# Kernel tuning notes

Measured on AMD Instinct MI355X. Metric: run time of the kernel, lower is better.

The kernel has to match this reference:

```python
import jax, jax.numpy as jnp
import numpy as np

EPS = 1e-12  # torch F.normalize default eps


def setup_inputs() -> dict:
    key = jax.random.key(0)
    ks = jax.random.split(key, 5)
    b, c, h, w = 2, 192, 256, 256
    x = jax.random.normal(ks[0], (b, c, h, w), dtype=jnp.float32)
    temperature = jnp.ones((1, 1, 1), dtype=jnp.float32)
    qkv_w = jax.random.normal(ks[1], (3 * c, c), dtype=jnp.float32) * 0.02
    qkv_b = jax.random.normal(ks[2], (3 * c,), dtype=jnp.float32) * 0.02
    proj_w = jax.random.normal(ks[3], (c, c), dtype=jnp.float32) * 0.02
    proj_b = jax.random.normal(ks[4], (c,), dtype=jnp.float32) * 0.02
    return {"x": x, "temperature": temperature, "qkv_w": qkv_w, "qkv_b": qkv_b,
            "proj_w": proj_w, "proj_b": proj_b}


def reference(x, temperature, qkv_w, qkv_b, proj_w, proj_b):
    b, c, h, w = x.shape
    n = h * w
    # [b, c, h, w] -> [b, n, c] tokens over spatial, features = channels
    xt = x.reshape(b, c, n).transpose(0, 2, 1)
    qkv = xt @ qkv_w.T + qkv_b                     # [b, n, 3c]
    q, k, v = jnp.split(qkv, 3, axis=-1)           # each [b, n, c]
    q = q.transpose(0, 2, 1)                       # [b, c, n]
    k = k.transpose(0, 2, 1)
    v = v.transpose(0, 2, 1)
    # L2 normalize along spatial (last) dim, torch-style clamp
    q = q / jnp.maximum(jnp.linalg.norm(q, axis=-1, keepdims=True), EPS)
    k = k / jnp.maximum(jnp.linalg.norm(k, axis=-1, keepdims=True), EPS)
    attn = jnp.einsum('bcn,bdn->bcd', q, k) * temperature[0, 0, 0]  # [b, c, c]
    attn = jax.nn.softmax(attn, axis=-1)
    out = jnp.einsum('bcd,bdn->bcn', attn, v)      # [b, c, n]
    out = out.reshape(b, c, h, w)
    # 1x1 conv projection = channel matmul
    out = jnp.einsum('bchw,dc->bdhw', out, proj_w) + proj_b[None, :, None, None]
    return out
```

## Files before the change

kernel.cpp:

```cpp
#include <hip/hip_runtime.h>
#include <hip/hip_bf16.h>
#include <stdint.h>

typedef __attribute__((ext_vector_type(8))) __bf16 bf16x8;
typedef __attribute__((ext_vector_type(4))) float f32x4;
typedef __attribute__((ext_vector_type(4))) uint u32x4;

#define C192 192
#define NSP 65536
#define EPS_N 1e-12f

#define SLICE_ELEMS 20224
#define ONES_OFF_E 19968

__device__ __forceinline__ uint32_t f2bf1(float a){
  uint32_t u = __float_as_uint(a);
  return (u + 0x7fffu + ((u >> 16) & 1u)) >> 16;
}
__device__ __forceinline__ uint32_t f2bf2(float lo, float hi){
  return f2bf1(lo) | (f2bf1(hi) << 16);
}
__device__ __forceinline__ float bf2f(ushort u){
  return __uint_as_float(((uint32_t)u) << 16);
}

__global__ __launch_bounds__(384, 2) void k_gram(const float* __restrict__ x,
                                                 ushort* __restrict__ gpart){
  __shared__ ushort xs[192 * 128];
  char* lb = (char*)xs;
  const int tid = threadIdx.x;
  const int lane = tid & 63, wid = tid >> 6;
  const int l15 = lane & 15, hi = lane >> 4;
  const int b = blockIdx.x >> 9, slice = blockIdx.x & 511;
  const int j0 = slice * 128;

  const int rA = wid, rB = 11 - wid, nA = 13 - rA;

  const float* xg = x + ((size_t)b * C192) * NSP + j0;

  float4 rf[16];
  #pragma unroll
  for (int u = 0; u < 8; u++){
    int unit = u * 384 + tid;
    int row = unit >> 4, u16 = unit & 15;
    const float* src = xg + (size_t)row * NSP + u16 * 8;
    rf[2 * u]     = *(const float4*)(src);
    rf[2 * u + 1] = *(const float4*)(src + 4);
  }
  #pragma unroll
  for (int u = 0; u < 8; u++){
    int unit = u * 384 + tid;
    int row = unit >> 4, u16 = unit & 15;
    uint4 v;
    v.x = f2bf2(rf[2 * u].x,     rf[2 * u].y);
    v.y = f2bf2(rf[2 * u].z,     rf[2 * u].w);
    v.z = f2bf2(rf[2 * u + 1].x, rf[2 * u + 1].y);
    v.w = f2bf2(rf[2 * u + 1].z, rf[2 * u + 1].w);
    int byte = row * 256 + u16 * 16; byte ^= (row & 7) << 4;
    *(uint4*)(lb + byte) = v;
  }

  f32x4 acc[15];
  #pragma unroll
  for (int t = 0; t < 15; t++) acc[t] = (f32x4){0.f, 0.f, 0.f, 0.f};

  __syncthreads();

  uint ov = (l15 == 0) ? 0x3F803F80u : 0u;
  u32x4 oq = {ov, ov, ov, ov};
  bf16x8 onesf = __builtin_bit_cast(bf16x8, oq);
  #pragma unroll
  for (int ks = 0; ks < 4; ks++){
    bf16x8 aA, aB;
    { int byte = (rA * 16 + l15) * 256 + ks * 64 + hi * 16; byte ^= (l15 & 7) << 4;
      aA = *(const bf16x8*)(lb + byte); }
    { int byte = (rB * 16 + l15) * 256 + ks * 64 + hi * 16; byte ^= (l15 & 7) << 4;
      aB = *(const bf16x8*)(lb + byte); }
    #pragma unroll
    for (int t = 0; t < 15; t++){
      int j = (t < nA) ? (rA + t) : (rB + t - nA);
      bf16x8 bf;
      if (j < 12){
        int byte = (j * 16 + l15) * 256 + ks * 64 + hi * 16; byte ^= (l15 & 7) << 4;
        bf = *(const bf16x8*)(lb + byte);
      } else {
        bf = onesf;
      }
      acc[t] = __builtin_amdgcn_mfma_f32_16x16x32_bf16((t < nA) ? aA : aB, bf, acc[t], 0, 0, 0);
    }
  }

  ushort* gp = gpart + (size_t)(b * 512 + slice) * SLICE_ELEMS;
  #pragma unroll
  for (int t = 0; t < 15; t++){
    int i = (t < nA) ? rA : rB;
    int j = (t < nA) ? (rA + t) : (rB + t - nA);
    uint2 u2;
    u2.x = f2bf2(acc[t][0], acc[t][1]);
    u2.y = f2bf2(acc[t][2], acc[t][3]);
    if (j < 12){
      int F = 12 * i - (i * (i - 1)) / 2 + (j - i);
      *(uint2*)(gp + F * 256 + lane * 4) = u2;
    } else if (l15 == 0){
      *(uint2*)(gp + ONES_OFF_E + i * 16 + hi * 4) = u2;
    }
  }
}

__global__ __launch_bounds__(1024) void k_reduce(const ushort* __restrict__ gpart,
                                                 float* __restrict__ gaug,
                                                 const float* __restrict__ qkv_w,
                                                 float* __restrict__ wkT){
  int blk = blockIdx.x, tid = threadIdx.x;
  if (blk < 180){
    __shared__ float red[4][256];
    int b = blk / 90, slot = blk % 90;
    int q = tid >> 8, e = tid & 255;
    float sum = 0.f;
    if (slot < 78){
      const ushort* p = gpart + (size_t)(b * 512 + q) * SLICE_ELEMS + slot * 256 + e;
      #pragma unroll 8
      for (int k2 = 0; k2 < 128; k2++) sum += bf2f(p[(size_t)k2 * (4 * SLICE_ELEMS)]);
    } else if (e < 16){
      int i = slot - 78;
      const ushort* p = gpart + (size_t)(b * 512 + q) * SLICE_ELEMS + ONES_OFF_E + i * 16 + e;
      #pragma unroll 8
      for (int k2 = 0; k2 < 128; k2++) sum += bf2f(p[(size_t)k2 * (4 * SLICE_ELEMS)]);
    }
    red[q][e] = sum;
    __syncthreads();
    if (tid < 256){
      float tot = red[0][tid] + red[1][tid] + red[2][tid] + red[3][tid];
      if (slot < 78){
        int i = 0, off = 0;
        while (slot >= off + (12 - i)){ off += 12 - i; i++; }
        int j = i + (slot - off);
        int e2 = tid;
        int row = ((e2 >> 6) << 2) | (e2 & 3);
        int col = (e2 >> 2) & 15;
        int R = i * 16 + row, Cc = j * 16 + col;
        gaug[((size_t)b * C192 + R) * 193 + Cc] = tot;
        gaug[((size_t)b * C192 + Cc) * 193 + R] = tot;
      } else if (tid < 16){
        int i = slot - 78;
        gaug[((size_t)b * C192 + i * 16 + tid) * 193 + 192] = tot;
      }
    }
  } else {
    int idx = (blk - 180) * 1024 + tid;
    if (idx < 36864){
      int d = idx / 192, e = idx % 192;
      wkT[e * 192 + d] = qkv_w[(192 + d) * 192 + e];
    }
  }
}

__global__ __launch_bounds__(256) void k_pr(const float* __restrict__ gaug,
                                            const float* __restrict__ qkv_w,
                                            const float* __restrict__ qkv_b,
                                            float* __restrict__ pr,
                                            float* __restrict__ norms){
  __shared__ float red[4];
  __shared__ float uSh;
  int blk = blockIdx.x, tid = threadIdx.x;
  int b = blk / 384, which = (blk / 192) % 2, c = blk % 192;
  const float* wrow = qkv_w + (which * 192 + c) * 192;
  float acc = 0.f;
  if (tid < 193){
    const float* g = gaug + (size_t)b * C192 * 193 + tid;
    #pragma unroll 4
    for (int e = 0; e < 192; e++) acc += wrow[e] * g[(size_t)e * 193];
    pr[(((size_t)b * 2 + which) * 192 + c) * 193 + tid] = acc;
  }
  if (tid == 192) uSh = acc;
  float v = (tid < 192) ? acc * wrow[tid] : 0.f;
  for (int o = 32; o > 0; o >>= 1) v += __shfl_down(v, o, 64);
  if ((tid & 63) == 0) red[tid >> 6] = v;
  __syncthreads();
  if (tid == 0){
    float s = red[0] + red[1] + red[2] + red[3];
    float bias = qkv_b[which * 192 + c];
    float n2 = s + 2.f * bias * uSh + 65536.f * bias * bias;
    norms[(b * 2 + which) * 192 + c] = fmaxf(sqrtf(fmaxf(n2, 0.f)), EPS_N);
  }
}

__global__ __launch_bounds__(256) void k_attn_u(const float* __restrict__ pr,
                                                const float* __restrict__ wkT,
                                                const float* __restrict__ norms,
                                                const float* __restrict__ qkv_b,
                                                const float* __restrict__ temperature,
                                                const float* __restrict__ qkv_w,
                                                float* __restrict__ uaug){
  __shared__ float Pc[193];
  __shared__ float red[4];
  __shared__ float bcast;
  int blk = blockIdx.x, tid = threadIdx.x;
  int b = blk / 192, c = blk % 192;
  if (tid < 193) Pc[tid] = pr[(((size_t)b * 2 + 0) * 192 + c) * 193 + tid];
  __syncthreads();
  int d = tid;
  float logit = -1e30f, p = 0.f;
  if (d < 192){
    float sS = 0.f;
    #pragma unroll 4
    for (int e = 0; e < 192; e++) sS += Pc[e] * wkT[e * 192 + d];
    float bq = qkv_b[c], bk = qkv_b[192 + d];
    float w2 = pr[(((size_t)b * 2 + 1) * 192 + d) * 193 + 192];
    float Sv = sS + Pc[192] * bk + bq * w2 + 65536.f * bq * bk;
    float nq = norms[(b * 2 + 0) * 192 + c];
    float nk = norms[(b * 2 + 1) * 192 + d];
    logit = temperature[0] * Sv / (nq * nk);
  }
  float m = logit;
  for (int o = 32; o > 0; o >>= 1) m = fmaxf(m, __shfl_down(m, o, 64));
  if ((tid & 63) == 0) red[tid >> 6] = m;
  __syncthreads();
  if (tid == 0) bcast = fmaxf(fmaxf(red[0], red[1]), fmaxf(red[2], red[3]));
  __syncthreads();
  m = bcast;
  p = (d < 192) ? __expf(logit - m) : 0.f;
  float s = p;
  for (int o = 32; o > 0; o >>= 1) s += __shfl_down(s, o, 64);
  __syncthreads();
  if ((tid & 63) == 0) red[tid >> 6] = s;
  __syncthreads();
  if (tid == 0) bcast = red[0] + red[1] + red[2] + red[3];
  __syncthreads();
  float aw = (d < 192) ? (p / bcast) : 0.f;
  __syncthreads();
  if (d < 192) Pc[d] = aw;
  __syncthreads();
  int e = tid;
  if (e <= 192){
    float acc = 0.f;
    if (e < 192){
      #pragma unroll 4
      for (int d2 = 0; d2 < 192; d2++) acc += Pc[d2] * qkv_w[(384 + d2) * 192 + e];
    } else {
      #pragma unroll 4
      for (int d2 = 0; d2 < 192; d2++) acc += Pc[d2] * qkv_b[384 + d2];
    }
    uaug[((size_t)b * 192 + c) * 193 + e] = acc;
  }
}

__global__ __launch_bounds__(256) void k_f(const float* __restrict__ uaug,
                                           const float* __restrict__ proj_w,
                                           const float* __restrict__ proj_b,
                                           ushort* __restrict__ fb,
                                           float* __restrict__ gvec){
  __shared__ float pw[192];
  int blk = blockIdx.x, tid = threadIdx.x;
  int b = blk / 192, f = blk % 192;
  if (tid < 192) pw[tid] = proj_w[f * 192 + tid];
  __syncthreads();
  int e = tid;
  if (e <= 192){
    float acc = 0.f;
    const float* u = uaug + (size_t)b * 192 * 193 + e;
    #pragma unroll 4
    for (int c2 = 0; c2 < 192; c2++) acc += pw[c2] * u[(size_t)c2 * 193];
    if (e < 192) fb[((size_t)b * 192 + f) * 192 + e] = (ushort)f2bf1(acc);
    else gvec[b * 192 + f] = acc + proj_b[f];
  }
}

__global__ __launch_bounds__(256, 3) void k_out(const float* __restrict__ x,
                                                const ushort* __restrict__ fb,
                                                const float* __restrict__ gvec,
                                                float* __restrict__ out){
  __shared__ ushort xt[128 * 192];
  char* lb = (char*)xt;
  const int tid = threadIdx.x;
  const int lane = tid & 63, wid = tid >> 6;
  const int l15 = lane & 15, hi = lane >> 4;
  const int b = blockIdx.x >> 9, cb = blockIdx.x & 511;
  const int j0 = cb * 128;

  const float* xg = x + ((size_t)b * C192) * NSP + j0;
  #pragma unroll
  for (int half = 0; half < 2; half++){
    float4 ra[12];
    #pragma unroll
    for (int ii = 0; ii < 3; ii++){
      int unit = (half * 3 + ii) * 256 + tid;
      int cp = unit >> 4, s8 = unit & 15;
      int c0 = cp * 2, sp0 = s8 * 8;
      const float* r0 = xg + (size_t)c0 * NSP + sp0;
      const float* r1 = xg + (size_t)(c0 + 1) * NSP + sp0;
      ra[4 * ii]     = *(const float4*)(r0);
      ra[4 * ii + 1] = *(const float4*)(r0 + 4);
      ra[4 * ii + 2] = *(const float4*)(r1);
      ra[4 * ii + 3] = *(const float4*)(r1 + 4);
    }
    #pragma unroll
    for (int ii = 0; ii < 3; ii++){
      int unit = (half * 3 + ii) * 256 + tid;
      int cp = unit >> 4, s8 = unit & 15;
      int c0 = cp * 2, sp0 = s8 * 8;
      float fa[8] = {ra[4*ii].x, ra[4*ii].y, ra[4*ii].z, ra[4*ii].w,
                     ra[4*ii+1].x, ra[4*ii+1].y, ra[4*ii+1].z, ra[4*ii+1].w};
      float fc[8] = {ra[4*ii+2].x, ra[4*ii+2].y, ra[4*ii+2].z, ra[4*ii+2].w,
                     ra[4*ii+3].x, ra[4*ii+3].y, ra[4*ii+3].z, ra[4*ii+3].w};
      #pragma unroll
      for (int s = 0; s < 8; s++){
        int sp = sp0 + s;
        int byte = sp * 384 + c0 * 2;
        byte ^= (((sp & 7) ^ ((sp >> 3) & 7)) << 4);
        *(uint*)(lb + byte) = f2bf2(fa[s], fc[s]);
      }
    }
  }

  float gfr[3][4];
  #pragma unroll
  for (int i = 0; i < 3; i++)
    #pragma unroll
    for (int r = 0; r < 4; r++)
      gfr[i][r] = gvec[b * 192 + (wid * 3 + i) * 16 + hi * 4 + r];

  f32x4 acc[3][8];
  #pragma unroll
  for (int i = 0; i < 3; i++)
    #pragma unroll
    for (int j = 0; j < 8; j++)
      acc[i][j] = (f32x4){0.f, 0.f, 0.f, 0.f};

  __syncthreads();

  for (int w = 0; w < 6; w++){
    bf16x8 aF[3];
    #pragma unroll
    for (int i = 0; i < 3; i++){
      const ushort* fr = fb + ((size_t)b * 192 + (wid * 3 + i) * 16 + l15) * 192;
      aF[i] = *(const bf16x8*)(fr + w * 32 + hi * 8);
    }
    #pragma unroll
    for (int ct = 0; ct < 8; ct++){
      int sp = ct * 16 + l15;
      int byte = sp * 384 + w * 64 + hi * 16;
      byte ^= (((sp & 7) ^ ((sp >> 3) & 7)) << 4);
      bf16x8 bf = *(const bf16x8*)(lb + byte);
      #pragma unroll
      for (int i = 0; i < 3; i++)
        acc[i][ct] = __builtin_amdgcn_mfma_f32_16x16x32_bf16(aF[i], bf, acc[i][ct], 0, 0, 0);
    }
  }

  #pragma unroll
  for (int i = 0; i < 3; i++){
    int row0 = (wid * 3 + i) * 16 + hi * 4;
    #pragma unroll
    for (int ct = 0; ct < 8; ct++){
      int sp = j0 + ct * 16 + l15;
      float* ob = out + ((size_t)b * C192 + row0) * NSP + sp;
      #pragma unroll
      for (int r = 0; r < 4; r++) ob[(size_t)r * NSP] = acc[i][ct][r] + gfr[i][r];
    }
  }
}

extern "C" void kernel_launch(void* const* d_in, const int* in_sizes, int n_in,
                              void* d_out, int out_size, void* d_ws, size_t ws_size,
                              hipStream_t stream){
  const float* x           = (const float*)d_in[0];
  const float* temperature = (const float*)d_in[1];
  const float* qkv_w       = (const float*)d_in[2];
  const float* qkv_b       = (const float*)d_in[3];
  const float* proj_w      = (const float*)d_in[4];
  const float* proj_b      = (const float*)d_in[5];
  float* out = (float*)d_out;
  char* ws = (char*)d_ws;

  ushort* gpart = (ushort*)(ws);
  float*  gaug  = (float*) (ws + 41418752);
  float*  pr    = (float*) (ws + 41715200);
  float*  wkT   = (float*) (ws + 42308096);
  float*  norms = (float*) (ws + 42455552);
  float*  uaug  = (float*) (ws + 42458624);
  ushort* fb    = (ushort*)(ws + 42755072);
  float*  gvec  = (float*) (ws + 42902528);

  hipLaunchKernelGGL(k_gram,   dim3(1024), dim3(384),  0, stream, x, gpart);
  hipLaunchKernelGGL(k_reduce, dim3(216),  dim3(1024), 0, stream, gpart, gaug, qkv_w, wkT);
  hipLaunchKernelGGL(k_pr,     dim3(768),  dim3(256),  0, stream, gaug, qkv_w, qkv_b, pr, norms);
  hipLaunchKernelGGL(k_attn_u, dim3(384),  dim3(256),  0, stream, pr, wkT, norms, qkv_b, temperature, qkv_w, uaug);
  hipLaunchKernelGGL(k_f,      dim3(384),  dim3(256),  0, stream, uaug, proj_w, proj_b, fb, gvec);
  hipLaunchKernelGGL(k_out,    dim3(1024), dim3(256),  0, stream, x, fb, gvec, out);
}
```

Before: 147.7 us.

## Pipeline Gram kernel with async global-to-LDS double buffering over wider slices

The Gram kernel now has each block process a 512-column slice in 16 chunks. Chunks are staged as fp32 into double-buffered LDS via global_load_lds, overlapping loads with MFMA compute, and converted to bf16 at fragment-load time. Work is split across 12 waves instead of 6, and there are 4x fewer partial slices, which shrinks the workspace and the reduce kernel's loop. The trade-offs are a per-chunk barrier, more conversion work per fragment read, fewer total blocks (256), and a higher launch bound that may pressure registers.

```diff
diff --git a/kernel.cpp b/kernel.cpp
--- a/kernel.cpp
+++ b/kernel.cpp
@@ -24,77 +24,81 @@
   return __uint_as_float(((uint32_t)u) << 16);
 }
 
-__global__ __launch_bounds__(384, 2) void k_gram(const float* __restrict__ x,
+__global__ __launch_bounds__(768, 4) void k_gram(const float* __restrict__ x,
                                                  ushort* __restrict__ gpart){
-  __shared__ ushort xs[192 * 128];
+  __shared__ float xs[2 * 6144];
   char* lb = (char*)xs;
   const int tid = threadIdx.x;
   const int lane = tid & 63, wid = tid >> 6;
   const int l15 = lane & 15, hi = lane >> 4;
-  const int b = blockIdx.x >> 9, slice = blockIdx.x & 511;
-  const int j0 = slice * 128;
-
-  const int rA = wid, rB = 11 - wid, nA = 13 - rA;
-
+  const int b = blockIdx.x >> 7, slice = blockIdx.x & 127;
+  const int j0 = slice * 512;
+
+  const int p = (wid < 6) ? wid : (wid - 6);
+  const int nFirst = 5 - p;
   const float* xg = x + ((size_t)b * C192) * NSP + j0;
 
-  float4 rf[16];
-  #pragma unroll
-  for (int u = 0; u < 8; u++){
-    int unit = u * 384 + tid;
-    int row = unit >> 4, u16 = unit & 15;
-    const float* src = xg + (size_t)row * NSP + u16 * 8;
-    rf[2 * u]     = *(const float4*)(src);
-    rf[2 * u + 1] = *(const float4*)(src + 4);
-  }
-  #pragma unroll
-  for (int u = 0; u < 8; u++){
-    int unit = u * 384 + tid;
-    int row = unit >> 4, u16 = unit & 15;
-    uint4 v;
-    v.x = f2bf2(rf[2 * u].x,     rf[2 * u].y);
-    v.y = f2bf2(rf[2 * u].z,     rf[2 * u].w);
-    v.z = f2bf2(rf[2 * u + 1].x, rf[2 * u + 1].y);
-    v.w = f2bf2(rf[2 * u + 1].z, rf[2 * u + 1].w);
-    int byte = row * 256 + u16 * 16; byte ^= (row & 7) << 4;
-    *(uint4*)(lb + byte) = v;
-  }
-
-  f32x4 acc[15];
-  #pragma unroll
-  for (int t = 0; t < 15; t++) acc[t] = (f32x4){0.f, 0.f, 0.f, 0.f};
-
-  __syncthreads();
+  const int swcol = ((lane & 7) ^ (lane >> 3)) * 4;
+  const float* srow = xg + (size_t)(wid * 16 + (lane >> 3)) * NSP + swcol;
+
+  auto ISSUE = [&](int c, int bi){
+    char* dst = lb + bi * 24576 + wid * 2048;
+    const float* s0 = srow + c * 32;
+    const float* s1 = s0 + (size_t)8 * NSP;
+    __builtin_amdgcn_global_load_lds((__attribute__((address_space(1))) const void*)s0,
+                                     (__attribute__((address_space(3))) void*)(dst), 16, 0, 0);
+    __builtin_amdgcn_global_load_lds((__attribute__((address_space(1))) const void*)s1,
+                                     (__attribute__((address_space(3))) void*)(dst + 1024), 16, 0, 0);
+  };
+
+  f32x4 acc[8];
+  #pragma unroll
+  for (int t = 0; t < 8; t++) acc[t] = (f32x4){0.f, 0.f, 0.f, 0.f};
 
   uint ov = (l15 == 0) ? 0x3F803F80u : 0u;
   u32x4 oq = {ov, ov, ov, ov};
   bf16x8 onesf = __builtin_bit_cast(bf16x8, oq);
-  #pragma unroll
-  for (int ks = 0; ks < 4; ks++){
-    bf16x8 aA, aB;
-    { int byte = (rA * 16 + l15) * 256 + ks * 64 + hi * 16; byte ^= (l15 & 7) << 4;
-      aA = *(const bf16x8*)(lb + byte); }
-    { int byte = (rB * 16 + l15) * 256 + ks * 64 + hi * 16; byte ^= (l15 & 7) << 4;
-      aB = *(const bf16x8*)(lb + byte); }
-    #pragma unroll
-    for (int t = 0; t < 15; t++){
-      int j = (t < nA) ? (rA + t) : (rB + t - nA);
-      bf16x8 bf;
-      if (j < 12){
-        int byte = (j * 16 + l15) * 256 + ks * 64 + hi * 16; byte ^= (l15 & 7) << 4;
-        bf = *(const bf16x8*)(lb + byte);
-      } else {
-        bf = onesf;
-      }
-      acc[t] = __builtin_amdgcn_mfma_f32_16x16x32_bf16((t < nA) ? aA : aB, bf, acc[t], 0, 0, 0);
-    }
-  }
-
-  ushort* gp = gpart + (size_t)(b * 512 + slice) * SLICE_ELEMS;
-  #pragma unroll
-  for (int t = 0; t < 15; t++){
-    int i = (t < nA) ? rA : rB;
-    int j = (t < nA) ? (rA + t) : (rB + t - nA);
+
+  auto LOADFRAG = [&](const char* base, int row) -> bf16x8 {
+    int sw = (row & 7) << 4;
+    f32x4 v0 = *(const f32x4*)(base + row * 128 + ((hi * 32) ^ sw));
+    f32x4 v1 = *(const f32x4*)(base + row * 128 + ((hi * 32 + 16) ^ sw));
+    uint w0, w1, w2, w3;
+    asm("v_cvt_pk_bf16_f32 %0, %1, %2" : "=v"(w0) : "v"(v0.x), "v"(v0.y));
+    asm("v_cvt_pk_bf16_f32 %0, %1, %2" : "=v"(w1) : "v"(v0.z), "v"(v0.w));
+    asm("v_cvt_pk_bf16_f32 %0, %1, %2" : "=v"(w2) : "v"(v1.x), "v"(v1.y));
+    asm("v_cvt_pk_bf16_f32 %0, %1, %2" : "=v"(w3) : "v"(v1.z), "v"(v1.w));
+    u32x4 q = {w0, w1, w2, w3};
+    return __builtin_bit_cast(bf16x8, q);
+  };
+
+  auto COMPUTE = [&](int bi){
+    const char* base = lb + bi * 24576;
+    bf16x8 a0 = LOADFRAG(base, p * 16 + l15);
+    bf16x8 a1 = (wid >= 6) ? LOADFRAG(base, (11 - p) * 16 + l15) : a0;
+    #pragma unroll
+    for (int t = 0; t < 8; t++){
+      if (wid >= 6 && t >= 7) break;
+      int j = (wid < 6) ? (p + t) : ((t < nFirst) ? (p + 8 + t) : (t + 6));
+      bf16x8 bf = (j < 12) ? LOADFRAG(base, j * 16 + l15) : onesf;
+      bf16x8 aS = (wid < 6 || t < nFirst) ? a0 : a1;
+      acc[t] = __builtin_amdgcn_mfma_f32_16x16x32_bf16(aS, bf, acc[t], 0, 0, 0);
+    }
+  };
+
+  ISSUE(0, 0);
+  for (int c = 0; c < 16; c++){
+    __syncthreads();
+    if (c < 15) ISSUE(c + 1, (c + 1) & 1);
+    COMPUTE(c & 1);
+  }
+
+  ushort* gp = gpart + (size_t)(b * 128 + slice) * SLICE_ELEMS;
+  #pragma unroll
+  for (int t = 0; t < 8; t++){
+    if (wid >= 6 && t >= 7) break;
+    int i = (wid < 6) ? p : ((t < nFirst) ? p : (11 - p));
+    int j = (wid < 6) ? (p + t) : ((t < nFirst) ? (p + 8 + t) : (t + 6));
     uint2 u2;
     u2.x = f2bf2(acc[t][0], acc[t][1]);
     u2.y = f2bf2(acc[t][2], acc[t][3]);
@@ -118,14 +122,14 @@
     int q = tid >> 8, e = tid & 255;
     float sum = 0.f;
     if (slot < 78){
-      const ushort* p = gpart + (size_t)(b * 512 + q) * SLICE_ELEMS + slot * 256 + e;
+      const ushort* pp = gpart + (size_t)(b * 128 + q) * SLICE_ELEMS + slot * 256 + e;
       #pragma unroll 8
-      for (int k2 = 0; k2 < 128; k2++) sum += bf2f(p[(size_t)k2 * (4 * SLICE_ELEMS)]);
+      for (int k2 = 0; k2 < 32; k2++) sum += bf2f(pp[(size_t)k2 * (4 * SLICE_ELEMS)]);
     } else if (e < 16){
       int i = slot - 78;
-      const ushort* p = gpart + (size_t)(b * 512 + q) * SLICE_ELEMS + ONES_OFF_E + i * 16 + e;
+      const ushort* pp = gpart + (size_t)(b * 128 + q) * SLICE_ELEMS + ONES_OFF_E + i * 16 + e;
       #pragma unroll 8
-      for (int k2 = 0; k2 < 128; k2++) sum += bf2f(p[(size_t)k2 * (4 * SLICE_ELEMS)]);
+      for (int k2 = 0; k2 < 32; k2++) sum += bf2f(pp[(size_t)k2 * (4 * SLICE_ELEMS)]);
     }
     red[q][e] = sum;
     __syncthreads();
@@ -200,7 +204,7 @@
   if (tid < 193) Pc[tid] = pr[(((size_t)b * 2 + 0) * 192 + c) * 193 + tid];
   __syncthreads();
   int d = tid;
-  float logit = -1e30f, p = 0.f;
+  float logit = -1e30f, pv = 0.f;
   if (d < 192){
     float sS = 0.f;
     #pragma unroll 4
@@ -219,15 +223,15 @@
   if (tid == 0) bcast = fmaxf(fmaxf(red[0], red[1]), fmaxf(red[2], red[3]));
   __syncthreads();
   m = bcast;
-  p = (d < 192) ? __expf(logit - m) : 0.f;
-  float s = p;
+  pv = (d < 192) ? __expf(logit - m) : 0.f;
+  float s = pv;
   for (int o = 32; o > 0; o >>= 1) s += __shfl_down(s, o, 64);
   __syncthreads();
   if ((tid & 63) == 0) red[tid >> 6] = s;
   __syncthreads();
   if (tid == 0) bcast = red[0] + red[1] + red[2] + red[3];
   __syncthreads();
-  float aw = (d < 192) ? (p / bcast) : 0.f;
+  float aw = (d < 192) ? (pv / bcast) : 0.f;
   __syncthreads();
   if (d < 192) Pc[d] = aw;
   __syncthreads();
@@ -374,15 +378,15 @@
   char* ws = (char*)d_ws;
 
   ushort* gpart = (ushort*)(ws);
-  float*  gaug  = (float*) (ws + 41418752);
-  float*  pr    = (float*) (ws + 41715200);
-  float*  wkT   = (float*) (ws + 42308096);
-  float*  norms = (float*) (ws + 42455552);
-  float*  uaug  = (float*) (ws + 42458624);
-  ushort* fb    = (ushort*)(ws + 42755072);
-  float*  gvec  = (float*) (ws + 42902528);
-
-  hipLaunchKernelGGL(k_gram,   dim3(1024), dim3(384),  0, stream, x, gpart);
+  float*  gaug  = (float*) (ws + 10354688);
+  float*  pr    = (float*) (ws + 10651136);
+  float*  wkT   = (float*) (ws + 11244032);
+  float*  norms = (float*) (ws + 11391488);
+  float*  uaug  = (float*) (ws + 11394560);
+  ushort* fb    = (ushort*)(ws + 11691008);
+  float*  gvec  = (float*) (ws + 11838464);
+
+  hipLaunchKernelGGL(k_gram,   dim3(256),  dim3(768),  0, stream, x, gpart);
   hipLaunchKernelGGL(k_reduce, dim3(216),  dim3(1024), 0, stream, gpart, gaug, qkv_w, wkT);
   hipLaunchKernelGGL(k_pr,     dim3(768),  dim3(256),  0, stream, gaug, qkv_w, qkv_b, pr, norms);
   hipLaunchKernelGGL(k_attn_u, dim3(384),  dim3(256),  0, stream, pr, wkT, norms, qkv_b, temperature, qkv_w, uaug);
```

Result: faster. 126.3 us (-14.5%).
